# Performance work log

Hardware: AMD Instinct MI355X
Metric: run time of the kernel (lower is better)

The kernel has to match this reference:

```python
import jax, jax.numpy as jnp
import numpy as np

PAD = 0          # pad_token_id == blank_index in the source module
NEG = -1e30      # log-space 'zero' (safe for fp32)


def _ctc_mean_loss(labels, logits, logits_mask):
    """Faithful jnp port of CTCLoss.call: tf.nn.ctc_loss (alpha forward DP,
    blank=pad, dense labels, logits [B,T,V]) + feasibility mask + mean."""
    B, T, V = logits.shape
    L = labels.shape[1]
    S = 2 * L + 1

    labels_len = jnp.sum(labels != PAD, axis=-1).astype(jnp.int32)   # [B]
    logits_len = jnp.sum(logits_mask, axis=-1).astype(jnp.int32)     # [B]

    logp = jax.nn.log_softmax(logits.astype(jnp.float32), axis=-1)   # [B,T,V]

    # Blank-interleaved extended label sequence: (blank, l1, blank, l2, ..., blank)
    ext = jnp.full((B, S), PAD, dtype=labels.dtype)
    ext = ext.at[:, 1::2].set(labels)                                # [B,S]
    ext_m2 = jnp.pad(ext, ((0, 0), (2, 0)), constant_values=PAD)[:, :S]
    allow_skip = (ext != PAD) & (ext != ext_m2)                      # [B,S]

    # Emission log-probs gathered at extended labels: em[b,t,s] = logp[b,t,ext[b,s]]
    em = jnp.take_along_axis(logp, jnp.broadcast_to(ext[:, None, :], (B, T, S)), axis=2)
    em = em.transpose(1, 0, 2)                                       # [T,B,S]

    neg = jnp.float32(NEG)
    alpha0 = jnp.full((B, S), neg, dtype=jnp.float32)
    alpha0 = alpha0.at[:, 0].set(em[0, :, 0]).at[:, 1].set(em[0, :, 1])

    t_idx = jnp.arange(1, T, dtype=jnp.int32)
    active = t_idx[:, None] < logits_len[None, :]                    # [T-1,B]

    def step(alpha, inp):
        em_t, act = inp                                              # [B,S], [B]
        p1 = jnp.concatenate([jnp.full((B, 1), neg), alpha[:, :-1]], axis=1)
        p2 = jnp.concatenate([jnp.full((B, 2), neg), alpha[:, :-2]], axis=1)
        p2 = jnp.where(allow_skip, p2, neg)
        new = em_t + jnp.logaddexp(jnp.logaddexp(alpha, p1), p2)
        alpha = jnp.where(act[:, None], new, alpha)                  # freeze past logit_len
        return alpha, None

    alpha, _ = jax.lax.scan(step, alpha0, (em[1:], active))          # [B,S]

    e = 2 * labels_len                                               # end of extended seq
    a_end = jnp.take_along_axis(alpha, e[:, None], axis=1)[:, 0]
    a_end1 = jnp.take_along_axis(alpha, jnp.maximum(e - 1, 0)[:, None], axis=1)[:, 0]
    loss = -jnp.logaddexp(a_end, a_end1)                             # per-example NLL

    loss_mask = (labels_len <= logits_len).astype(jnp.float32)
    return jnp.mean(loss * loss_mask)


def setup_inputs() -> dict:
    key = jax.random.key(0)
    k1, k2, k3, k4 = jax.random.split(key, 4)
    B, T, V, L = 256, 1024, 64, 64

    lab_len = jax.random.randint(k1, (B,), L // 2, L + 1)            # [32,64]
    vals = jax.random.randint(k2, (B, L), 1, V)                      # non-blank tokens
    labels = jnp.where(jnp.arange(L)[None, :] < lab_len[:, None], vals, 0).astype(jnp.int64)

    log_len = jax.random.randint(k3, (B,), 2 * L + 64, T + 1)        # feasible alignments
    logits_mask = jnp.arange(T)[None, :] < log_len[:, None]          # prefix-True mask

    logits = jax.random.normal(k4, (B, T, V), dtype=jnp.float32)
    return {"labels": labels, "logits": logits, "logits_mask": logits_mask}


def reference(labels, logits, logits_mask):
    return _ctc_mean_loss(labels, logits, logits_mask)
```

## Files before the change

kernel.cpp:

```cpp
#include <hip/hip_runtime.h>

#define BB 256
#define TT 1024
#define VV 64
#define LL 64
#define LOG2E 1.4426950408889634f
#define LN2   0.6931471805599453f

__device__ __forceinline__ int   f2i(float x) { return __float_as_int(x); }
__device__ __forceinline__ float i2f(int x)   { return __int_as_float(x); }

__device__ __forceinline__ void barrier_lds() {
  asm volatile("s_waitcnt lgkmcnt(0)" ::: "memory");
  __builtin_amdgcn_s_barrier();
}

__device__ __forceinline__ float wave_max63(float x) {
  x = fmaxf(x, i2f(__builtin_amdgcn_update_dpp(0, f2i(x), 0x111, 0xF, 0xF, true)));
  x = fmaxf(x, i2f(__builtin_amdgcn_update_dpp(0, f2i(x), 0x112, 0xF, 0xF, true)));
  x = fmaxf(x, i2f(__builtin_amdgcn_update_dpp(0, f2i(x), 0x114, 0xF, 0xF, true)));
  x = fmaxf(x, i2f(__builtin_amdgcn_update_dpp(0, f2i(x), 0x118, 0xF, 0xF, true)));
  x = fmaxf(x, i2f(__builtin_amdgcn_update_dpp(0, f2i(x), 0x142, 0xF, 0xF, true)));
  x = fmaxf(x, i2f(__builtin_amdgcn_update_dpp(0, f2i(x), 0x143, 0xF, 0xF, true)));
  return i2f(__builtin_amdgcn_readlane(f2i(x), 63));
}

__device__ __forceinline__ void gload16(const float* g, float* l) {
  __builtin_amdgcn_global_load_lds(
      (const __attribute__((address_space(1))) unsigned int*)g,
      (__attribute__((address_space(3))) unsigned int*)l, 16, 0, 0);
}

extern "C" __global__ void __launch_bounds__(320, 1)
ctc_fused(const int* __restrict__ labels, const float* __restrict__ logits,
          const int* __restrict__ mask, float* __restrict__ out) {
  __shared__ __align__(16) float rawb[4][16][VV];
  __shared__ float lsePart[4];
  const int b = blockIdx.x;
  const int tid = threadIdx.x;
  const int lane = tid & 63;
  const int wv = tid >> 6;

  const float* lg = logits + (size_t)b * TT * VV;

  int lsum = 0;
  const int* mrow = mask + b * TT;
#pragma unroll
  for (int k = 0; k < TT / 64; ++k) lsum += mrow[lane + (k << 6)];
#pragma unroll
  for (int off = 32; off; off >>= 1) lsum += __shfl_xor(lsum, off);
  int len = __builtin_amdgcn_readfirstlane(lsum);
  len = len < 1 ? 1 : (len > TT ? TT : len);
  const int nwin = (len + 15) >> 4;

  int lab = 0, lab_len = 0;
  float sk = 0.0f;
  float A0 = 0.0f, A1 = 0.0f, A2 = 0.0f;
  int ctot = 0;
  if (wv == 0) {
    lab = labels[b * LL + lane] & 63;
    lab_len = (int)__popcll(__ballot(lab != 0));
    const int plab = __builtin_amdgcn_update_dpp(0, lab, 0x138, 0xF, 0xF, false);
    sk = (lab != 0 && lab != plab) ? 1.0f : 0.0f;
    A0 = (lane == 0) ? 1.0f : 0.0f;
    __builtin_amdgcn_s_setprio(1);
  }

  const int rg = lane >> 4;
  const int colv = (lane & 15) << 2;
  const int r0 = ((wv - 1) << 2) + rg;
  float acc = 0.0f;

#define GLOAD(WN) gload16(lg + (size_t)(((((WN) << 4) + ((wv - 1) << 2)) << 6) + (lane << 2)), \
                          &rawb[(WN) & 3][(wv - 1) << 2][0])

#define RENORM() { \
    const float mxv = wave_max63(fmaxf(fmaxf(A0, A1), A2)); \
    const int eb = (f2i(mxv) >> 23) & 255; \
    int kk = (eb > 0 && eb < 255) ? (187 - eb) : 0; \
    kk = kk > 126 ? 126 : (kk < -126 ? -126 : kk); \
    ctot += kk; \
    const float sc = i2f((127 + kk) << 23); \
    A0 *= sc; A1 *= sc; A2 *= sc; \
  }

#define STEPU(U) { \
    const float A1p = i2f(__builtin_amdgcn_update_dpp(0, f2i(A1), 0x138, 0xF, 0xF, false)); \
    const float nA0 = c##U * (A0 + A1p); \
    const float nA1 = g##U * fmaf(sk, A1p, A0 + A1); \
    A2 = c##U * (A2 + A1); \
    A0 = nA0; A1 = nA1; \
  }

#define STEPM(U) { \
    const float A1p = i2f(__builtin_amdgcn_update_dpp(0, f2i(A1), 0x138, 0xF, 0xF, false)); \
    const float nA0 = c##U * (A0 + A1p); \
    const float nA1 = g##U * fmaf(sk, A1p, A0 + A1); \
    const float nA2 = c##U * (A2 + A1); \
    const bool act = (tbase + (U)) < len; \
    A0 = act ? nA0 : A0; A1 = act ? nA1 : A1; A2 = act ? nA2 : A2; \
  }

  if (wv != 0) { GLOAD(0); GLOAD(1); GLOAD(2); }

  for (int w = 0; w < nwin; ++w) {
    if (wv != 0) {
      if (w < 62)       asm volatile("s_waitcnt vmcnt(2)" ::: "memory");
      else if (w == 62) asm volatile("s_waitcnt vmcnt(1)" ::: "memory");
      else              asm volatile("s_waitcnt vmcnt(0)" ::: "memory");
    }
    barrier_lds();
    if (wv != 0) {
      const int wn = w + 3;
      if (wn < 64) GLOAD(wn);
      const float4 rv = *(const float4*)&rawb[w & 3][r0][colv];
      const float e0 = __builtin_amdgcn_exp2f(rv.x * LOG2E);
      const float e1 = __builtin_amdgcn_exp2f(rv.y * LOG2E);
      const float e2 = __builtin_amdgcn_exp2f(rv.z * LOG2E);
      const float e3 = __builtin_amdgcn_exp2f(rv.w * LOG2E);
      float s = (e0 + e1) + (e2 + e3);
      s += i2f(__builtin_amdgcn_update_dpp(0, f2i(s), 0x111, 0xF, 0xF, true));
      s += i2f(__builtin_amdgcn_update_dpp(0, f2i(s), 0x112, 0xF, 0xF, true));
      s += i2f(__builtin_amdgcn_update_dpp(0, f2i(s), 0x114, 0xF, 0xF, true));
      s += i2f(__builtin_amdgcn_update_dpp(0, f2i(s), 0x118, 0xF, 0xF, true));
      if ((lane & 15) == 15 && (((w << 4) + r0) < len)) acc += __logf(s);
    } else {
      const float* rb = &rawb[w & 3][0][0];
      float c0, c1, c2, c3, c4, c5, c6, c7, c8, c9, c10, c11, c12, c13, c14, c15;
      float g0, g1, g2, g3, g4, g5, g6, g7, g8, g9, g10, g11, g12, g13, g14, g15;
#define RD(U) c##U = rb[(U) << 6]; g##U = rb[((U) << 6) + lab];
      RD(0)  RD(1)  RD(2)  RD(3)  RD(4)  RD(5)  RD(6)  RD(7)
      RD(8)  RD(9)  RD(10) RD(11) RD(12) RD(13) RD(14) RD(15)
#undef RD
      asm volatile("" ::: "memory");
#define EX(U) c##U = __builtin_amdgcn_exp2f(c##U * LOG2E); \
              g##U = __builtin_amdgcn_exp2f(g##U * LOG2E);
      EX(0)  EX(1)  EX(2)  EX(3)  EX(4)  EX(5)  EX(6)  EX(7)
      EX(8)  EX(9)  EX(10) EX(11) EX(12) EX(13) EX(14) EX(15)
#undef EX
      RENORM()
      const int tbase = w << 4;
      if (tbase + 16 <= len) {
        STEPU(0)  STEPU(1)  STEPU(2)  STEPU(3)  STEPU(4)  STEPU(5)  STEPU(6)  STEPU(7)
        STEPU(8)  STEPU(9)  STEPU(10) STEPU(11) STEPU(12) STEPU(13) STEPU(14) STEPU(15)
      } else {
        STEPM(0)  STEPM(1)  STEPM(2)  STEPM(3)  STEPM(4)  STEPM(5)  STEPM(6)  STEPM(7)
        STEPM(8)  STEPM(9)  STEPM(10) STEPM(11) STEPM(12) STEPM(13) STEPM(14) STEPM(15)
      }
    }
  }

  if (wv != 0) {
    asm volatile("s_waitcnt vmcnt(0)" ::: "memory");
    float a = ((lane & 15) == 15) ? acc : 0.0f;
    a += __shfl_xor(a, 16);
    a += __shfl_xor(a, 32);
    if (lane == 63) lsePart[wv - 1] = a;
  }
  barrier_lds();

  if (wv == 0) {
    float ae, ae1;
    if (lab_len >= LL) {
      ae  = i2f(__builtin_amdgcn_readlane(f2i(A2), 63));
      ae1 = i2f(__builtin_amdgcn_readlane(f2i(A1), 63));
    } else if (lab_len >= 1) {
      ae  = i2f(__builtin_amdgcn_readlane(f2i(A0), lab_len));
      ae1 = i2f(__builtin_amdgcn_readlane(f2i(A1), lab_len - 1));
    } else {
      ae  = i2f(__builtin_amdgcn_readlane(f2i(A0), 0));
      ae1 = ae;
    }
    const float se = ae + ae1;
    float loss = ((lsePart[0] + lsePart[1]) + (lsePart[2] + lsePart[3]))
               - LN2 * (__builtin_amdgcn_logf(se) - (float)ctot);
    if (lab_len > len) loss = 0.0f;
    if (lane == 0) atomicAdd(out, loss * (1.0f / 256.0f));
  }
#undef STEPM
#undef STEPU
#undef RENORM
#undef GLOAD
}

extern "C" void kernel_launch(void* const* d_in, const int* in_sizes, int n_in,
                              void* d_out, int out_size, void* d_ws, size_t ws_size,
                              hipStream_t stream) {
  (void)in_sizes; (void)n_in; (void)out_size; (void)d_ws; (void)ws_size;
  hipMemsetAsync(d_out, 0, sizeof(float), stream);
  ctc_fused<<<dim3(BB), dim3(320), 0, stream>>>(
      (const int*)d_in[0], (const float*)d_in[1], (const int*)d_in[2], (float*)d_out);
}
```

Baseline: 133.9 us.

## Use single producer wave with register prefetch and shared exp buffer

Replaces the four producer waves that used global-to-LDS async loads with one producer wave. That wave prefetches logits into registers several windows ahead, computes exp once, and writes the exponentials to a double-buffered LDS tile. The DP wave then reads precomputed exp values instead of recomputing 32 exp2 per window. This shrinks the block to 128 threads and removes redundant exp work on the serial critical path. In exchange, one wave now carries all softmax and load work, which could become the bottleneck.

```diff
diff --git a/kernel.cpp b/kernel.cpp
--- a/kernel.cpp
+++ b/kernel.cpp
@@ -25,17 +25,12 @@
   return i2f(__builtin_amdgcn_readlane(f2i(x), 63));
 }
 
-__device__ __forceinline__ void gload16(const float* g, float* l) {
-  __builtin_amdgcn_global_load_lds(
-      (const __attribute__((address_space(1))) unsigned int*)g,
-      (__attribute__((address_space(3))) unsigned int*)l, 16, 0, 0);
-}
-
-extern "C" __global__ void __launch_bounds__(320, 1)
+extern "C" __global__ void __launch_bounds__(128, 1)
 ctc_fused(const int* __restrict__ labels, const float* __restrict__ logits,
           const int* __restrict__ mask, float* __restrict__ out) {
-  __shared__ __align__(16) float rawb[4][16][VV];
-  __shared__ float lsePart[4];
+  __shared__ __align__(16) float ebuf[2][16][VV];
+  __shared__ __align__(16) float cexpb[2][16];
+  __shared__ float lsePart;
   const int b = blockIdx.x;
   const int tid = threadIdx.x;
   const int lane = tid & 63;
@@ -66,18 +61,45 @@
     __builtin_amdgcn_s_setprio(1);
   }
 
-  const int rg = lane >> 4;
-  const int colv = (lane & 15) << 2;
-  const int r0 = ((wv - 1) << 2) + rg;
+  const int prow = lane >> 4;
+  const int pcol = (lane & 15) << 2;
+  const float* gbase = lg + (size_t)(prow * VV) + pcol;
   float acc = 0.0f;
 
-#define GLOAD(WN) gload16(lg + (size_t)(((((WN) << 4) + ((wv - 1) << 2)) << 6) + (lane << 2)), \
-                          &rawb[(WN) & 3][(wv - 1) << 2][0])
+  float4 ra0{0,0,0,0}, ra1{0,0,0,0}, ra2{0,0,0,0}, ra3{0,0,0,0};
+  float4 rb0{0,0,0,0}, rb1{0,0,0,0}, rb2{0,0,0,0}, rb3{0,0,0,0};
+  float4 rc0{0,0,0,0}, rc1{0,0,0,0}, rc2{0,0,0,0}, rc3{0,0,0,0};
+
+#define ISSUE(WN, S) { \
+    const float* p_ = gbase + ((WN) << 10); \
+    S##0 = *(const float4*)(p_); \
+    S##1 = *(const float4*)(p_ + 256); \
+    S##2 = *(const float4*)(p_ + 512); \
+    S##3 = *(const float4*)(p_ + 768); \
+  }
+
+#define PEMIT(WN, LD, V) { \
+    const float e0 = __builtin_amdgcn_exp2f((V).x * LOG2E); \
+    const float e1 = __builtin_amdgcn_exp2f((V).y * LOG2E); \
+    const float e2 = __builtin_amdgcn_exp2f((V).z * LOG2E); \
+    const float e3 = __builtin_amdgcn_exp2f((V).w * LOG2E); \
+    float4 ev; ev.x = e0; ev.y = e1; ev.z = e2; ev.w = e3; \
+    *(float4*)&ebuf[(WN) & 1][((LD) << 2) + prow][pcol] = ev; \
+    if ((lane & 15) == 0) cexpb[(WN) & 1][((LD) << 2) + prow] = e0; \
+    float s = (e0 + e1) + (e2 + e3); \
+    s += i2f(__builtin_amdgcn_update_dpp(0, f2i(s), 0x111, 0xF, 0xF, true)); \
+    s += i2f(__builtin_amdgcn_update_dpp(0, f2i(s), 0x112, 0xF, 0xF, true)); \
+    s += i2f(__builtin_amdgcn_update_dpp(0, f2i(s), 0x114, 0xF, 0xF, true)); \
+    s += i2f(__builtin_amdgcn_update_dpp(0, f2i(s), 0x118, 0xF, 0xF, true)); \
+    if ((lane & 15) == 15 && ((((WN) << 4) + ((LD) << 2) + prow) < len)) acc += __logf(s); \
+  }
+
+#define PRODUCE(WN, S) { PEMIT(WN, 0, S##0) PEMIT(WN, 1, S##1) PEMIT(WN, 2, S##2) PEMIT(WN, 3, S##3) }
 
 #define RENORM() { \
     const float mxv = wave_max63(fmaxf(fmaxf(A0, A1), A2)); \
-    const int eb = (f2i(mxv) >> 23) & 255; \
-    int kk = (eb > 0 && eb < 255) ? (187 - eb) : 0; \
+    const int eb_ = (f2i(mxv) >> 23) & 255; \
+    int kk = (eb_ > 0 && eb_ < 255) ? (187 - eb_) : 0; \
     kk = kk > 126 ? 126 : (kk < -126 ? -126 : kk); \
     ctot += kk; \
     const float sc = i2f((127 + kk) << 23); \
@@ -101,61 +123,58 @@
     A0 = act ? nA0 : A0; A1 = act ? nA1 : A1; A2 = act ? nA2 : A2; \
   }
 
-  if (wv != 0) { GLOAD(0); GLOAD(1); GLOAD(2); }
-
-  for (int w = 0; w < nwin; ++w) {
-    if (wv != 0) {
-      if (w < 62)       asm volatile("s_waitcnt vmcnt(2)" ::: "memory");
-      else if (w == 62) asm volatile("s_waitcnt vmcnt(1)" ::: "memory");
-      else              asm volatile("s_waitcnt vmcnt(0)" ::: "memory");
-    }
-    barrier_lds();
-    if (wv != 0) {
-      const int wn = w + 3;
-      if (wn < 64) GLOAD(wn);
-      const float4 rv = *(const float4*)&rawb[w & 3][r0][colv];
-      const float e0 = __builtin_amdgcn_exp2f(rv.x * LOG2E);
-      const float e1 = __builtin_amdgcn_exp2f(rv.y * LOG2E);
-      const float e2 = __builtin_amdgcn_exp2f(rv.z * LOG2E);
-      const float e3 = __builtin_amdgcn_exp2f(rv.w * LOG2E);
-      float s = (e0 + e1) + (e2 + e3);
-      s += i2f(__builtin_amdgcn_update_dpp(0, f2i(s), 0x111, 0xF, 0xF, true));
-      s += i2f(__builtin_amdgcn_update_dpp(0, f2i(s), 0x112, 0xF, 0xF, true));
-      s += i2f(__builtin_amdgcn_update_dpp(0, f2i(s), 0x114, 0xF, 0xF, true));
-      s += i2f(__builtin_amdgcn_update_dpp(0, f2i(s), 0x118, 0xF, 0xF, true));
-      if ((lane & 15) == 15 && (((w << 4) + r0) < len)) acc += __logf(s);
-    } else {
-      const float* rb = &rawb[w & 3][0][0];
-      float c0, c1, c2, c3, c4, c5, c6, c7, c8, c9, c10, c11, c12, c13, c14, c15;
-      float g0, g1, g2, g3, g4, g5, g6, g7, g8, g9, g10, g11, g12, g13, g14, g15;
-#define RD(U) c##U = rb[(U) << 6]; g##U = rb[((U) << 6) + lab];
-      RD(0)  RD(1)  RD(2)  RD(3)  RD(4)  RD(5)  RD(6)  RD(7)
-      RD(8)  RD(9)  RD(10) RD(11) RD(12) RD(13) RD(14) RD(15)
-#undef RD
-      asm volatile("" ::: "memory");
-#define EX(U) c##U = __builtin_amdgcn_exp2f(c##U * LOG2E); \
-              g##U = __builtin_amdgcn_exp2f(g##U * LOG2E);
-      EX(0)  EX(1)  EX(2)  EX(3)  EX(4)  EX(5)  EX(6)  EX(7)
-      EX(8)  EX(9)  EX(10) EX(11) EX(12) EX(13) EX(14) EX(15)
-#undef EX
-      RENORM()
-      const int tbase = w << 4;
-      if (tbase + 16 <= len) {
-        STEPU(0)  STEPU(1)  STEPU(2)  STEPU(3)  STEPU(4)  STEPU(5)  STEPU(6)  STEPU(7)
-        STEPU(8)  STEPU(9)  STEPU(10) STEPU(11) STEPU(12) STEPU(13) STEPU(14) STEPU(15)
-      } else {
-        STEPM(0)  STEPM(1)  STEPM(2)  STEPM(3)  STEPM(4)  STEPM(5)  STEPM(6)  STEPM(7)
-        STEPM(8)  STEPM(9)  STEPM(10) STEPM(11) STEPM(12) STEPM(13) STEPM(14) STEPM(15)
-      }
-    }
+#define CONSUME(W) { \
+    const float* eb = &ebuf[(W) & 1][0][0]; \
+    float g0,g1,g2,g3,g4,g5,g6,g7,g8,g9,g10,g11,g12,g13,g14,g15; \
+    g0  = eb[(0<<6)  + lab]; g1  = eb[(1<<6)  + lab]; g2  = eb[(2<<6)  + lab]; g3  = eb[(3<<6)  + lab]; \
+    g4  = eb[(4<<6)  + lab]; g5  = eb[(5<<6)  + lab]; g6  = eb[(6<<6)  + lab]; g7  = eb[(7<<6)  + lab]; \
+    g8  = eb[(8<<6)  + lab]; g9  = eb[(9<<6)  + lab]; g10 = eb[(10<<6) + lab]; g11 = eb[(11<<6) + lab]; \
+    g12 = eb[(12<<6) + lab]; g13 = eb[(13<<6) + lab]; g14 = eb[(14<<6) + lab]; g15 = eb[(15<<6) + lab]; \
+    const float4* cp = (const float4*)cexpb[(W) & 1]; \
+    const float4 cva = cp[0], cvb = cp[1], cvc = cp[2], cvd = cp[3]; \
+    const float c0 = cva.x,  c1 = cva.y,  c2 = cva.z,  c3 = cva.w; \
+    const float c4 = cvb.x,  c5 = cvb.y,  c6 = cvb.z,  c7 = cvb.w; \
+    const float c8 = cvc.x,  c9 = cvc.y,  c10 = cvc.z, c11 = cvc.w; \
+    const float c12 = cvd.x, c13 = cvd.y, c14 = cvd.z, c15 = cvd.w; \
+    RENORM() \
+    const int tbase = (W) << 4; \
+    if (tbase + 16 <= len) { \
+      STEPU(0)  STEPU(1)  STEPU(2)  STEPU(3)  STEPU(4)  STEPU(5)  STEPU(6)  STEPU(7) \
+      STEPU(8)  STEPU(9)  STEPU(10) STEPU(11) STEPU(12) STEPU(13) STEPU(14) STEPU(15) \
+    } else { \
+      STEPM(0)  STEPM(1)  STEPM(2)  STEPM(3)  STEPM(4)  STEPM(5)  STEPM(6)  STEPM(7) \
+      STEPM(8)  STEPM(9)  STEPM(10) STEPM(11) STEPM(12) STEPM(13) STEPM(14) STEPM(15) \
+    } \
+  }
+
+#define BODY(W, S) { \
+    barrier_lds(); \
+    if (wv != 0) { \
+      if ((W) + 1 < 64) { PRODUCE((W) + 1, S) } \
+      if ((W) + 4 < 64) { ISSUE((W) + 4, S) } \
+    } else { \
+      CONSUME(W) \
+    } \
   }
 
   if (wv != 0) {
-    asm volatile("s_waitcnt vmcnt(0)" ::: "memory");
+    ISSUE(0, ra) ISSUE(1, rb) ISSUE(2, rc)
+    PRODUCE(0, ra)
+    ISSUE(3, ra)
+  }
+
+  int w = 0;
+  for (; w + 3 <= nwin; w += 3) {
+    BODY(w, rb) BODY(w + 1, rc) BODY(w + 2, ra)
+  }
+  if (w < nwin) { BODY(w, rb) ++w; }
+  if (w < nwin) { BODY(w, rc) ++w; }
+
+  if (wv != 0) {
     float a = ((lane & 15) == 15) ? acc : 0.0f;
     a += __shfl_xor(a, 16);
     a += __shfl_xor(a, 32);
-    if (lane == 63) lsePart[wv - 1] = a;
+    if (lane == 63) lsePart = a;
   }
   barrier_lds();
 
@@ -172,15 +191,19 @@
       ae1 = ae;
     }
     const float se = ae + ae1;
-    float loss = ((lsePart[0] + lsePart[1]) + (lsePart[2] + lsePart[3]))
+    float loss = lsePart
                - LN2 * (__builtin_amdgcn_logf(se) - (float)ctot);
     if (lab_len > len) loss = 0.0f;
     if (lane == 0) atomicAdd(out, loss * (1.0f / 256.0f));
   }
+#undef BODY
+#undef CONSUME
 #undef STEPM
 #undef STEPU
 #undef RENORM
-#undef GLOAD
+#undef PRODUCE
+#undef PEMIT
+#undef ISSUE
 }
 
 extern "C" void kernel_launch(void* const* d_in, const int* in_sizes, int n_in,
@@ -188,6 +211,6 @@
                               hipStream_t stream) {
   (void)in_sizes; (void)n_in; (void)out_size; (void)d_ws; (void)ws_size;
   hipMemsetAsync(d_out, 0, sizeof(float), stream);
-  ctc_fused<<<dim3(BB), dim3(320), 0, stream>>>(
+  ctc_fused<<<dim3(BB), dim3(128), 0, stream>>>(
       (const int*)d_in[0], (const float*)d_in[1], (const int*)d_in[2], (float*)d_out);
 }
```

Measured after the change: 148.1 us. 10.6% more time.
